# Kernel optimization log

Hardware: AMD Instinct MI355X
Metric: run time of the kernel (lower is better)

## Reference

```python
import jax, jax.numpy as jnp
import numpy as np

DN = ('NCDHW', 'OIDHW', 'NCDHW')


def conv3(x, w):
    # 3x3x3 'same' conv (submanifold conv on a dense volume == padded dense conv)
    return jax.lax.conv_general_dilated(x, w, (1, 1, 1), [(1, 1)] * 3, dimension_numbers=DN)


def conv1(x, w):
    # 1x1x1 conv
    return jax.lax.conv_general_dilated(x, w, (1, 1, 1), 'VALID', dimension_numbers=DN)


def avg_pool(x, ksz):
    s = jax.lax.reduce_window(x, 0.0, jax.lax.add, (1, 1) + ksz, (1, 1) + ksz, 'VALID')
    return s / float(np.prod(ksz))


def setup_inputs() -> dict:
    key = jax.random.key(0)
    ks = jax.random.split(key, 14)
    B, C, D, H, W = 1, 64, 48, 64, 128
    n_dense = 5  # nconvs - 1

    def he(k, shape, fan):
        return jax.random.normal(k, shape, jnp.float32) * np.sqrt(2.0 / fan).astype(np.float32)

    return {
        'fvl': jax.random.normal(ks[0], (B, C, D, H, W), jnp.float32),
        'w_a1': he(ks[1], (C, C, 3, 3, 3), 27 * C),
        'w_a2': he(ks[2], (C, C, 3, 3, 3), 27 * C),
        'w_nin': he(ks[3], (C, C, 1, 1, 1), C),
        'w1s': he(ks[4], (n_dense, C, C, 1, 1, 1), C),
        'w2s': he(ks[5], (n_dense, C, C, 1, 1, 1), C),
        'wp0': he(ks[6], (C, C, 1, 1, 1), C),
        'wp1': he(ks[7], (C, C, 1, 1, 1), C),
        'wp2': he(ks[8], (C, C, 1, 1, 1), C),
        'wp3': he(ks[9], (C, C, 1, 1, 1), C),
        'wc1': he(ks[10], (C, C, 3, 3, 3), 27 * C),
        'wc2': he(ks[11], (1, C, 3, 3, 3), 27 * 1),
        'bc': jnp.zeros((1,), jnp.float32),
    }


def reference(fvl, w_a1, w_a2, w_nin, w1s, w2s, wp0, wp1, wp2, wp3, wc1, wc2, bc):
    # --- Conv3dBlock_sparse: (conv3 -> conv3) + NIN(1x1), summed (no relu) ---
    x = conv3(conv3(fvl, w_a1), w_a2) + conv1(fvl, w_nin)
    # --- (nconvs-1) dense 1x1x1 residual blocks: relu(conv1(x) + conv2(conv1(x))) ---
    for i in range(w1s.shape[0]):
        x1 = conv1(x, w1s[i])
        x2 = conv1(x1, w2s[i])
        x = jax.nn.relu(x1 + x2)
    # --- PSP-style multi-scale pool pyramid ---
    B, C, d, h, w = x.shape
    pool_ws = [wp0, wp1, wp2, wp3]
    out_sum = x
    for i, ps in enumerate(np.linspace(1, min(d, h, w) // 2, 4, dtype=int)):
        ksz = (int(d / ps), int(h / ps), int(w / ps))
        o = avg_pool(x, ksz)
        o = conv1(o, pool_ws[i])
        o = jax.image.resize(o, (B, C, d, h, w), method='trilinear')  # align_corners=False semantics
        out_sum = out_sum + 0.25 * o
    x = jax.nn.relu(out_sum / 2.0)
    # --- classify head (eval path, up=False): conv3 -> relu -> conv3(+bias) ---
    c = conv3(jax.nn.relu(conv3(x, wc1)), wc2) + bc.reshape(1, -1, 1, 1, 1)
    return (x, jnp.squeeze(c, 1))
```

## Files before the change

### kernel.cpp

```cpp
#include <hip/hip_runtime.h>
#include <math.h>

#define DD 48
#define HH 64
#define WW 128
#define VOL (DD*HH*WW)
#define PW 130
#define PROWS (DD*HH)
#define PVOL (PROWS*PW)
#define PVBYTES ((long)PVOL*64*2)
#define GUARD 16640L
#define NC 64

typedef __attribute__((ext_vector_type(8))) short bf16x8;
typedef __attribute__((ext_vector_type(4))) float f32x4;
typedef __attribute__((ext_vector_type(4))) unsigned int u32x4v;
typedef __attribute__((ext_vector_type(2))) unsigned int u32x2v;

__device__ __forceinline__ float bflo(unsigned int u){
    union { unsigned int i; float f; } x; x.i = u<<16; return x.f; }
__device__ __forceinline__ float bfhi(unsigned int u){
    union { unsigned int i; float f; } x; x.i = u & 0xffff0000u; return x.f; }
__device__ __forceinline__ float bf2f(unsigned short u){
    union { unsigned int i; float f; } x; x.i = ((unsigned int)u)<<16; return x.f; }
__device__ __forceinline__ unsigned short f2bf(float f){
    union { float f; unsigned int i; } x; x.f = f;
    unsigned int i = x.i;
    return (unsigned short)((i + 0x7fffu + ((i>>16)&1u)) >> 16);
}

__device__ __forceinline__ void gload16(const void* g, void* l){
    __builtin_amdgcn_global_load_lds(
        (const __attribute__((address_space(1))) void*)g,
        (__attribute__((address_space(3))) void*)l, 16, 0, 0);
}

__global__ void k_prep_all(
    const float* __restrict__ w_a1, const float* __restrict__ w_a2,
    const float* __restrict__ wc1,  const float* __restrict__ wnin,
    const float* __restrict__ wc2,  const float* __restrict__ w1s,
    const float* __restrict__ w2s,  const float* __restrict__ wp1,
    const float* __restrict__ wp2,  const float* __restrict__ wp3,
    unsigned short* __restrict__ wa1t, unsigned short* __restrict__ wa2t,
    unsigned short* __restrict__ wc1t, unsigned short* __restrict__ nint,
    unsigned short* __restrict__ wt2,  unsigned short* __restrict__ Mt,
    float* __restrict__ wpt)
{
    int b = blockIdx.x, tid = threadIdx.x;
    if (b < 1296){
        int which = b/432, bb = b - which*432;
        int idx = bb*256 + tid;
        if (idx < 27*64*64){
            const float* src = which==0 ? w_a1 : (which==1 ? w_a2 : wc1);
            unsigned short* dst = which==0 ? wa1t : (which==1 ? wa2t : wc1t);
            int ci = idx & 63; int t = idx >> 6; int co = t & 63; int k = t >> 6;
            dst[idx] = f2bf(src[(co*64+ci)*27 + k]);
        }
    } else if (b < 1376){
        int idx = (b-1296)*256 + tid;
        int i = idx >> 12; int r = idx & 4095;
        int co = r >> 6; int ci = r & 63;
        const float* W1 = w1s + i*4096;
        const float* W2 = w2s + i*4096;
        float m = W1[co*64+ci];
        for (int k=0;k<64;++k) m += W2[co*64+k]*W1[k*64+ci];
        Mt[idx] = f2bf(m);
    } else if (b < 1392){
        int idx = (b-1376)*256 + tid;
        nint[idx] = f2bf(wnin[idx]);
    } else if (b < 1400){
        int idx = (b-1392)*256 + tid;
        int co = idx & 63; int row = idx >> 6;
        float v = (row < 27) ? wc2[co*27 + row] : 0.f;
        wt2[row*64 + co] = f2bf(v);
    } else {
        int bb = b - 1400;
        int which = bb/16;
        int idx = (bb - which*16)*256 + tid;
        const float* src = which==0 ? wp1 : (which==1 ? wp2 : wp3);
        int ci = idx >> 6; int co = idx & 63;
        wpt[which*4096 + idx] = src[co*64+ci];
    }
}

__global__ __launch_bounds__(256) void k_zeropad(unsigned short* __restrict__ pv0,
                                                 unsigned short* __restrict__ pv1){
    int idx = blockIdx.x*256 + threadIdx.x;
    int seg = idx >> 3, part = idx & 7;
    int vol = seg / 6144; int r2 = seg - vol*6144;
    int row = r2 >> 1; int col = (r2 & 1) ? 129 : 0;
    long boff = ((long)row*130 + col)*128 + part*16;
    u32x4v z = {0,0,0,0};
    char* base = (char*)(vol ? pv1 : pv0);
    *(u32x4v*)(base + boff) = z;
}

__global__ __launch_bounds__(256) void k_tobf16v(const float* __restrict__ src,
                                                 unsigned short* __restrict__ dst){
    __shared__ unsigned short lds[64*66];
    int tid = threadIdx.x;
    long vbase = (long)blockIdx.x*64;
    int d = (int)(vbase >> 13);
    int h = (int)((vbase >> 7) & 63);
    int w0 = (int)(vbase & 127);
    long pbase = ((long)(d*64+h)*PW + w0 + 1);
    int v = tid & 63;
    int cg = tid >> 6;
#pragma unroll
    for (int k=0;k<16;++k){
        int ci = cg*16 + k;
        lds[v*66 + ci] = f2bf(src[(long)ci*VOL + vbase + v]);
    }
    __syncthreads();
#pragma unroll
    for (int it=0; it<2; ++it){
        int chunk = it*256 + tid;
        int vv = chunk >> 3, gp = chunk & 7;
        const unsigned short* s = lds + vv*66 + gp*8;
        unsigned int w0_ = (unsigned)s[0] | ((unsigned)s[1]<<16);
        unsigned int w1_ = (unsigned)s[2] | ((unsigned)s[3]<<16);
        unsigned int w2_ = (unsigned)s[4] | ((unsigned)s[5]<<16);
        unsigned int w3_ = (unsigned)s[6] | ((unsigned)s[7]<<16);
        u32x4v q = {w0_,w1_,w2_,w3_};
        *(u32x4v*)(dst + (pbase+vv)*64 + gp*8) = q;
    }
}

template<bool AUX, bool RELU>
__global__ __launch_bounds__(256,2) void k_conv3m(
    const unsigned short* __restrict__ in, const unsigned short* __restrict__ wt,
    const unsigned short* __restrict__ aux, const unsigned short* __restrict__ auxw,
    unsigned short* __restrict__ out)
{
    __shared__ __align__(16) char sA[36864];
    __shared__ __align__(16) char sB[33280];

    const int tid  = threadIdx.x;
    const int lane = tid & 63;
    const int wave = tid >> 6;
    const int ll = lane & 15;
    const int kg = lane >> 4;
    const int bid = blockIdx.x;
    const int wid = ((bid & 7) * 192) + (bid >> 3);
    const int vbr = wid*256;
    const int d  = vbr >> 13;
    const int h0 = (vbr >> 7) & 63;
    const int my_h  = h0 + (wave >> 1);
    const int my_w0 = (wave & 1) * 64;
    const long pvb = (long)(d*64 + my_h)*PW + my_w0 + 1;

    const char* inb = (const char*)in;
    const char* wtb = (const char*)wt;

    f32x4 acc[4][4];
#pragma unroll
    for (int a=0;a<4;++a)
#pragma unroll
        for (int b=0;b<4;++b) acc[a][b] = (f32x4){0.f,0.f,0.f,0.f};

#pragma unroll
    for (int kd=0; kd<3; ++kd){
        const int dd = d + kd - 1;
        if ((unsigned)dd >= 48u) continue;
        const long rowstart = ((long)(dd*64 + h0 - 1)) * 130;
#pragma unroll
        for (int khalf=0; khalf<2; ++khalf){
            __syncthreads();
#pragma unroll
            for (int rnd=0; rnd<9; ++rnd){
                int j = rnd*4096 + tid*16;
                int q = j ^ (((j>>7)&3)<<4);
                const char* src = wtb + (long)(kd*9 + (q>>12))*8192
                                      + (long)((q>>6)&63)*128 + khalf*64 + (q&63);
                gload16(src, sA + j);
            }
#pragma unroll
            for (int rnd=0; rnd<8; ++rnd){
                int j = rnd*4096 + tid*16;
                int q = j ^ (((j>>7)&3)<<4);
                const char* src = inb + (rowstart + (q>>6))*128 + khalf*64 + (q&63);
                gload16(src, sB + j);
            }
            if (tid < 32){
                int j = 32768 + tid*16;
                int q = j ^ (((j>>7)&3)<<4);
                const char* src = inb + (rowstart + (q>>6))*128 + khalf*64 + (q&63);
                gload16(src, sB + j);
            }
            __syncthreads();
#pragma unroll
            for (int kh=0; kh<3; ++kh){
                const int hh = my_h + kh - 1;
                if ((unsigned)hh >= 64u) continue;
                const int rr = (wave>>1) + kh;
#pragma unroll
                for (int kw=0; kw<3; ++kw){
                    const int tap_rel = kh*3 + kw;
                    bf16x8 Af[4], Bf[4];
#pragma unroll
                    for (int t=0;t<4;++t){
                        int qa = tap_rel*4096 + (t*16+ll)*64 + kg*16;
                        Af[t] = *(const bf16x8*)(sA + (qa ^ (((qa>>7)&3)<<4)));
                    }
#pragma unroll
                    for (int vt=0; vt<4; ++vt){
                        int vrel = rr*130 + my_w0 + vt*16 + ll + kw;
                        int qb = vrel*64 + kg*16;
                        Bf[vt] = *(const bf16x8*)(sB + (qb ^ (((qb>>7)&3)<<4)));
                    }
#pragma unroll
                    for (int vt=0; vt<4; ++vt)
#pragma unroll
                        for (int t=0; t<4; ++t)
                            acc[t][vt] = __builtin_amdgcn_mfma_f32_16x16x32_bf16(Af[t], Bf[vt], acc[t][vt], 0,0,0);
                }
            }
        }
    }

    if (AUX){
        bf16x8 Aa[2][4], Ba[2][4];
#pragma unroll
        for (int half=0; half<2; ++half){
            const int ko = half*32 + kg*8;
#pragma unroll
            for (int t=0;t<4;++t)
                Aa[half][t] = *(const bf16x8*)(auxw + (t*16+ll)*64 + ko);
#pragma unroll
            for (int vt=0; vt<4; ++vt)
                Ba[half][vt] = *(const bf16x8*)(aux + (pvb + vt*16 + ll)*64 + ko);
        }
#pragma unroll
        for (int half=0; half<2; ++half)
#pragma unroll
            for (int vt=0; vt<4; ++vt)
#pragma unroll
                for (int t=0;t<4;++t)
                    acc[t][vt] = __builtin_amdgcn_mfma_f32_16x16x32_bf16(Aa[half][t], Ba[half][vt], acc[t][vt], 0,0,0);
    }

#pragma unroll
    for (int vt=0; vt<4; ++vt){
        unsigned short* op = out + (pvb + vt*16 + ll)*64 + kg*4;
#pragma unroll
        for (int t=0;t<4;++t){
            float r0 = acc[t][vt][0], r1 = acc[t][vt][1], r2 = acc[t][vt][2], r3 = acc[t][vt][3];
            if (RELU){ r0=fmaxf(r0,0.f); r1=fmaxf(r1,0.f); r2=fmaxf(r2,0.f); r3=fmaxf(r3,0.f); }
            unsigned int lo = (unsigned)f2bf(r0) | ((unsigned)f2bf(r1)<<16);
            unsigned int hi = (unsigned)f2bf(r2) | ((unsigned)f2bf(r3)<<16);
            u32x2v q = {lo, hi};
            *(u32x2v*)(op + t*16) = q;
        }
    }
}

__global__ __launch_bounds__(256,2) void k_conv3h(
    const unsigned short* __restrict__ in, const unsigned short* __restrict__ wt,
    const unsigned short* __restrict__ wt2, unsigned short* __restrict__ t)
{
    __shared__ __align__(16) char sA[36864];
    __shared__ __align__(16) char sB[33280];

    const int tid  = threadIdx.x;
    const int lane = tid & 63;
    const int wave = tid >> 6;
    const int ll = lane & 15;
    const int kg = lane >> 4;
    const int bid = blockIdx.x;
    const int wid = ((bid & 7) * 192) + (bid >> 3);
    const int vbr = wid*256;
    const int d  = vbr >> 13;
    const int h0 = (vbr >> 7) & 63;
    const int my_h  = h0 + (wave >> 1);
    const int my_w0 = (wave & 1) * 64;
    const long pvb = (long)(d*64 + my_h)*PW + my_w0 + 1;

    const char* inb = (const char*)in;
    const char* wtb = (const char*)wt;

    f32x4 acc[4][4];
#pragma unroll
    for (int a=0;a<4;++a)
#pragma unroll
        for (int b=0;b<4;++b) acc[a][b] = (f32x4){0.f,0.f,0.f,0.f};

#pragma unroll
    for (int kd=0; kd<3; ++kd){
        const int dd = d + kd - 1;
        if ((unsigned)dd >= 48u) continue;
        const long rowstart = ((long)(dd*64 + h0 - 1)) * 130;
#pragma unroll
        for (int khalf=0; khalf<2; ++khalf){
            __syncthreads();
#pragma unroll
            for (int rnd=0; rnd<9; ++rnd){
                int j = rnd*4096 + tid*16;
                int q = j ^ (((j>>7)&3)<<4);
                const char* src = wtb + (long)(kd*9 + (q>>12))*8192
                                      + (long)((q>>6)&63)*128 + khalf*64 + (q&63);
                gload16(src, sA + j);
            }
#pragma unroll
            for (int rnd=0; rnd<8; ++rnd){
                int j = rnd*4096 + tid*16;
                int q = j ^ (((j>>7)&3)<<4);
                const char* src = inb + (rowstart + (q>>6))*128 + khalf*64 + (q&63);
                gload16(src, sB + j);
            }
            if (tid < 32){
                int j = 32768 + tid*16;
                int q = j ^ (((j>>7)&3)<<4);
                const char* src = inb + (rowstart + (q>>6))*128 + khalf*64 + (q&63);
                gload16(src, sB + j);
            }
            __syncthreads();
#pragma unroll
            for (int kh=0; kh<3; ++kh){
                const int hh = my_h + kh - 1;
                if ((unsigned)hh >= 64u) continue;
                const int rr = (wave>>1) + kh;
#pragma unroll
                for (int kw=0; kw<3; ++kw){
                    const int tap_rel = kh*3 + kw;
                    bf16x8 Af[4], Bf[4];
#pragma unroll
                    for (int tt=0;tt<4;++tt){
                        int qa = tap_rel*4096 + (tt*16+ll)*64 + kg*16;
                        Af[tt] = *(const bf16x8*)(sA + (qa ^ (((qa>>7)&3)<<4)));
                    }
#pragma unroll
                    for (int vt=0; vt<4; ++vt){
                        int vrel = rr*130 + my_w0 + vt*16 + ll + kw;
                        int qb = vrel*64 + kg*16;
                        Bf[vt] = *(const bf16x8*)(sB + (qb ^ (((qb>>7)&3)<<4)));
                    }
#pragma unroll
                    for (int vt=0; vt<4; ++vt)
#pragma unroll
                        for (int tt=0; tt<4; ++tt)
                            acc[tt][vt] = __builtin_amdgcn_mfma_f32_16x16x32_bf16(Af[tt], Bf[vt], acc[tt][vt], 0,0,0);
                }
            }
        }
    }

    __syncthreads();
    char* myL = sA + wave*8192;
#pragma unroll
    for (int vt=0; vt<4; ++vt){
        const int row = vt*16 + ll;
        const int sw = (row & 7) << 4;
#pragma unroll
        for (int tt=0;tt<4;++tt){
            float r0 = fmaxf(acc[tt][vt][0],0.f), r1 = fmaxf(acc[tt][vt][1],0.f);
            float r2 = fmaxf(acc[tt][vt][2],0.f), r3 = fmaxf(acc[tt][vt][3],0.f);
            unsigned int lo = (unsigned)f2bf(r0) | ((unsigned)f2bf(r1)<<16);
            unsigned int hi = (unsigned)f2bf(r2) | ((unsigned)f2bf(r3)<<16);
            u32x2v q = {lo, hi};
            int colb = kg*8 + tt*32;
            *(u32x2v*)(myL + row*128 + (colb ^ sw)) = q;
        }
    }
    f32x4 acc2[2][4];
#pragma unroll
    for (int a=0;a<2;++a)
#pragma unroll
        for (int b=0;b<4;++b) acc2[a][b] = (f32x4){0.f,0.f,0.f,0.f};
#pragma unroll
    for (int half=0; half<2; ++half){
        const int ko = half*32 + kg*8;
        bf16x8 afr[2];
#pragma unroll
        for (int tl=0;tl<2;++tl)
            afr[tl] = *(const bf16x8*)(wt2 + (tl*16+ll)*64 + ko);
#pragma unroll
        for (int vt=0; vt<4; ++vt){
            const int row = vt*16 + ll;
            const int sw = (row & 7) << 4;
            int colb = half*64 + kg*16;
            bf16x8 bfr = *(const bf16x8*)(myL + row*128 + (colb ^ sw));
#pragma unroll
            for (int tl=0;tl<2;++tl)
                acc2[tl][vt] = __builtin_amdgcn_mfma_f32_16x16x32_bf16(afr[tl], bfr, acc2[tl][vt], 0,0,0);
        }
    }
#pragma unroll
    for (int vt=0; vt<4; ++vt){
        long vx = pvb + vt*16 + ll;
#pragma unroll
        for (int tl=0;tl<2;++tl){
#pragma unroll
            for (int r=0;r<4;++r){
                int tap = tl*16 + kg*4 + r;
                if (tap < 27) t[(long)tap*PVOL + vx] = f2bf(acc2[tl][vt][r]);
            }
        }
    }
}

__global__ __launch_bounds__(256,3) void k_chain(const unsigned short* __restrict__ in,
        const unsigned short* __restrict__ Mt, unsigned short* __restrict__ out){
    __shared__ __align__(16) char sX[4][8192];
    const int lane = threadIdx.x & 63;
    const int wave = threadIdx.x >> 6;
    const int ll = lane & 15;
    const int kg = lane >> 4;
    const long vb = (long)blockIdx.x*256 + wave*64;
    char* myL = sX[wave];

    bf16x8 B[2][4];
#pragma unroll
    for (int half=0; half<2; ++half){
        const int ko = half*32 + kg*8;
#pragma unroll
        for (int vt=0; vt<4; ++vt)
            B[half][vt] = *(const bf16x8*)(in + (vb+vt*16+ll)*64 + ko);
    }

#pragma unroll
    for (int s=0; s<5; ++s){
        const unsigned short* wt = Mt + s*4096;
        bf16x8 A[2][4];
#pragma unroll
        for (int half=0; half<2; ++half){
            const int ko = half*32 + kg*8;
#pragma unroll
            for (int t=0;t<4;++t)
                A[half][t] = *(const bf16x8*)(wt + (t*16+ll)*64 + ko);
        }
        f32x4 acc[4][4];
#pragma unroll
        for (int a=0;a<4;++a)
#pragma unroll
            for (int b=0;b<4;++b) acc[a][b] = (f32x4){0.f,0.f,0.f,0.f};
#pragma unroll
        for (int half=0; half<2; ++half)
#pragma unroll
            for (int vt=0; vt<4; ++vt)
#pragma unroll
                for (int t=0;t<4;++t)
                    acc[t][vt] = __builtin_amdgcn_mfma_f32_16x16x32_bf16(A[half][t], B[half][vt], acc[t][vt], 0,0,0);

        if (s < 4){
#pragma unroll
            for (int vt=0; vt<4; ++vt){
                const int row = vt*16 + ll;
                const int sw = (row & 7) << 4;
#pragma unroll
                for (int t=0;t<4;++t){
                    float r0 = fmaxf(acc[t][vt][0],0.f), r1 = fmaxf(acc[t][vt][1],0.f);
                    float r2 = fmaxf(acc[t][vt][2],0.f), r3 = fmaxf(acc[t][vt][3],0.f);
                    unsigned int lo = (unsigned)f2bf(r0) | ((unsigned)f2bf(r1)<<16);
                    unsigned int hi = (unsigned)f2bf(r2) | ((unsigned)f2bf(r3)<<16);
                    u32x2v q = {lo, hi};
                    int colb = kg*8 + t*32;
                    *(u32x2v*)(myL + row*128 + (colb ^ sw)) = q;
                }
            }
#pragma unroll
            for (int half=0; half<2; ++half){
#pragma unroll
                for (int vt=0; vt<4; ++vt){
                    const int row = vt*16 + ll;
                    const int sw = (row & 7) << 4;
                    int colb = half*64 + kg*16;
                    B[half][vt] = *(const bf16x8*)(myL + row*128 + (colb ^ sw));
                }
            }
        } else {
#pragma unroll
            for (int vt=0; vt<4; ++vt){
                unsigned short* op = out + (vb+vt*16+ll)*64 + kg*4;
#pragma unroll
                for (int t=0;t<4;++t){
                    float r0 = fmaxf(acc[t][vt][0],0.f), r1 = fmaxf(acc[t][vt][1],0.f);
                    float r2 = fmaxf(acc[t][vt][2],0.f), r3 = fmaxf(acc[t][vt][3],0.f);
                    unsigned int lo = (unsigned)f2bf(r0) | ((unsigned)f2bf(r1)<<16);
                    unsigned int hi = (unsigned)f2bf(r2) | ((unsigned)f2bf(r3)<<16);
                    u32x2v q = {lo, hi};
                    *(u32x2v*)(op + t*16) = q;
                }
            }
        }
    }
}

__global__ __launch_bounds__(256) void k_heads(const unsigned short* __restrict__ t,
        const float* __restrict__ bias, float* __restrict__ out){
    int g = blockIdx.x*256 + threadIdx.x;
    int v0 = g*4;
    int w0 = v0 & 127; int h = (v0>>7)&63; int d = v0>>13;
    long p0 = (long)(d*64+h)*PW + w0 + 1;
    float b0 = bias[0];
    float s0=b0, s1=b0, s2=b0, s3=b0;
#pragma unroll
    for (int kd=0;kd<3;++kd){
#pragma unroll
      for (int kh=0;kh<3;++kh){
#pragma unroll
        for (int kw=0;kw<3;++kw){
            const int tap = (kd*3+kh)*3+kw;
            const long dvp = (long)((kd-1)*64 + (kh-1))*PW + (kw-1);
            bool okdh = ((unsigned)(d+kd-1)<48u) && ((unsigned)(h+kh-1)<64u);
            const unsigned short* tp = t + (long)tap*PVOL;
            bool ok0 = okdh && ((unsigned)(w0+0+kw-1)<128u);
            bool ok1 = okdh && ((unsigned)(w0+1+kw-1)<128u);
            bool ok2 = okdh && ((unsigned)(w0+2+kw-1)<128u);
            bool ok3 = okdh && ((unsigned)(w0+3+kw-1)<128u);
            long a0 = ok0 ? (p0+0+dvp) : p0;
            long a1 = ok1 ? (p0+1+dvp) : p0;
            long a2 = ok2 ? (p0+2+dvp) : p0;
            long a3 = ok3 ? (p0+3+dvp) : p0;
            float x0 = bf2f(tp[a0]);
            float x1 = bf2f(tp[a1]);
            float x2 = bf2f(tp[a2]);
            float x3 = bf2f(tp[a3]);
            s0 += ok0 ? x0 : 0.f;
            s1 += ok1 ? x1 : 0.f;
            s2 += ok2 ? x2 : 0.f;
            s3 += ok3 ? x3 : 0.f;
        }
      }
    }
    f32x4 r = {s0,s1,s2,s3};
    *(f32x4*)(out + v0) = r;
}

__global__ __launch_bounds__(256) void k_pool3(const unsigned short* __restrict__ in,
                                               float* __restrict__ S3){
    __shared__ float sm[32*68];
    int tid = threadIdx.x;
    int cg = tid & 7, part = tid >> 3;
    int cell = blockIdx.x;
    int Z = cell >> 8, Y = (cell >> 4) & 15, X = cell & 15;
    float a[8];
#pragma unroll
    for (int j=0;j<8;++j) a[j]=0.f;
#pragma unroll
    for (int j=0;j<3;++j){
        int i = part*3 + j;
        int di = i >> 5, rem = i & 31, hi = rem >> 3, wi = rem & 7;
        long p = ((long)((3*Z+di)*64 + 4*Y+hi))*PW + 8*X+wi + 1;
        u32x4v q = *(const u32x4v*)(in + p*64 + cg*8);
#pragma unroll
        for (int e=0;e<4;++e){ a[e*2] += bflo(q[e]); a[e*2+1] += bfhi(q[e]); }
    }
#pragma unroll
    for (int j=0;j<8;++j) sm[part*68 + cg*8 + j] = a[j];
    __syncthreads();
    if (tid < 64){
        float s=0.f;
        for (int r=0;r<32;++r) s += sm[r*68 + tid];
        S3[tid*4096 + cell] = s;
    }
}

__global__ __launch_bounds__(256) void k_pool2(const float* __restrict__ S3,
                                               float* __restrict__ P2){
    int idx = blockIdx.x*256 + threadIdx.x;
    int cell = idx & 511; int c = idx >> 9;
    int z = cell >> 6, y = (cell >> 3) & 7, x = cell & 7;
    const float* b = S3 + c*4096;
    float s = 0.f;
#pragma unroll
    for (int a2=0;a2<2;++a2)
#pragma unroll
        for (int b2=0;b2<2;++b2)
#pragma unroll
            for (int e=0;e<2;++e)
                s += b[((2*z+a2)<<8) + ((2*y+b2)<<4) + (2*x+e)];
    P2[c*512 + cell] = s;
}

__global__ void k_gcm(const float* __restrict__ S3, const float* __restrict__ wp0,
                      float* __restrict__ gc){
    __shared__ float sm[4][64];
    __shared__ float sg[64];
    int tid = threadIdx.x;
    int c = tid & 63, part = tid >> 6;
    float s = 0.f;
    const float* row = S3 + c*4096 + part*1024;
    for (int i=0;i<1024;i+=4){
        f32x4 q = *(const f32x4*)(row + i);
        s += q[0]+q[1]+q[2]+q[3];
    }
    sm[part][c] = s;
    __syncthreads();
    if (tid < 64){
        sg[tid] = (sm[0][tid]+sm[1][tid]+sm[2][tid]+sm[3][tid]) * (1.0f/(float)VOL);
    }
    __syncthreads();
    if (tid < 64){
        float g=0.f;
        for (int ci=0;ci<64;++ci) g += wp0[tid*64+ci]*sg[ci];
        gc[tid] = g;
    }
}

__global__ __launch_bounds__(256) void k_pool4(const unsigned short* __restrict__ in,
                                               float* __restrict__ P4){
    __shared__ float sm[32*68];
    int tid = threadIdx.x;
    int cg = tid & 7, part = (tid >> 3) & 3, slot = tid >> 5;
    int cell = blockIdx.x*8 + slot;
    int z = cell / 800; int rem = cell - z*800; int y = rem / 25; int x = rem - y*25;
    int a2 = part >> 1, b2 = part & 1;
    float a[8];
#pragma unroll
    for (int j=0;j<8;++j) a[j]=0.f;
#pragma unroll
    for (int e=0;e<5;++e){
        long p = ((long)((2*z+a2)*64 + 2*y+b2))*PW + 5*x+e + 1;
        u32x4v q = *(const u32x4v*)(in + p*64 + cg*8);
#pragma unroll
        for (int k=0;k<4;++k){ a[k*2] += bflo(q[k]); a[k*2+1] += bfhi(q[k]); }
    }
#pragma unroll
    for (int j=0;j<8;++j) sm[(slot*4+part)*68 + cg*8 + j] = a[j];
    __syncthreads();
#pragma unroll
    for (int r=0;r<2;++r){
        int o = r*256 + tid;
        int c = o >> 3, s = o & 7;
        float v = sm[(s*4+0)*68 + c] + sm[(s*4+1)*68 + c]
                + sm[(s*4+2)*68 + c] + sm[(s*4+3)*68 + c];
        P4[(long)c*19200 + blockIdx.x*8 + s] = v;
    }
}

__global__ void k_conv1(const float* __restrict__ in, const float* __restrict__ wt,
                        float* __restrict__ out, int vol, float scale){
    int v = blockIdx.x*256 + threadIdx.x;
    if (v >= vol) return;
    float acc[64];
#pragma unroll
    for (int i=0;i<64;++i) acc[i]=0.f;
    for (int ci=0; ci<64; ++ci){
        float xv = in[ci*vol + v];
        const float* wr = wt + ci*64;
#pragma unroll
        for (int co=0; co<64; ++co) acc[co] = fmaf(wr[co], xv, acc[co]);
    }
    float* op = out + (long)v*64;
#pragma unroll
    for (int q=0;q<16;++q){
        f32x4 t = {acc[q*4]*scale, acc[q*4+1]*scale, acc[q*4+2]*scale, acc[q*4+3]*scale};
        *(f32x4*)(op + q*4) = t;
    }
}

__device__ __forceinline__ void tri_setup(int d,int h,int w,int gd,int gh,int gw,
                                          int* o, float* wt){
    float fz = (d+0.5f)*((float)gd/(float)DD) - 0.5f;
    float fy = (h+0.5f)*((float)gh/(float)HH) - 0.5f;
    float fx = (w+0.5f)*((float)gw/(float)WW) - 0.5f;
    float z0f = floorf(fz), y0f = floorf(fy), x0f = floorf(fx);
    float tz = fz - z0f, ty = fy - y0f, tx = fx - x0f;
    int z0 = (int)z0f, y0 = (int)y0f, x0 = (int)x0f;
    int z1 = z0+1, y1 = y0+1, x1 = x0+1;
    z0 = min(max(z0,0),gd-1); z1 = min(max(z1,0),gd-1);
    y0 = min(max(y0,0),gh-1); y1 = min(max(y1,0),gh-1);
    x0 = min(max(x0,0),gw-1); x1 = min(max(x1,0),gw-1);
    o[0] = (z0*gh+y0)*gw+x0; wt[0] = (1-tz)*(1-ty)*(1-tx);
    o[1] = (z0*gh+y0)*gw+x1; wt[1] = (1-tz)*(1-ty)*tx;
    o[2] = (z0*gh+y1)*gw+x0; wt[2] = (1-tz)*ty*(1-tx);
    o[3] = (z0*gh+y1)*gw+x1; wt[3] = (1-tz)*ty*tx;
    o[4] = (z1*gh+y0)*gw+x0; wt[4] = tz*(1-ty)*(1-tx);
    o[5] = (z1*gh+y0)*gw+x1; wt[5] = tz*(1-ty)*tx;
    o[6] = (z1*gh+y1)*gw+x0; wt[6] = tz*ty*(1-tx);
    o[7] = (z1*gh+y1)*gw+x1; wt[7] = tz*ty*tx;
}

__global__ __launch_bounds__(512) void k_combine(
        const unsigned short* __restrict__ xc, const float* __restrict__ gc,
        const float* __restrict__ p2, const float* __restrict__ p3,
        const float* __restrict__ p4, float* __restrict__ xout,
        unsigned short* __restrict__ xv){
    int tid = threadIdx.x;
    const int bid = blockIdx.x;
    const int wid = ((bid & 7) * 96) + (bid >> 3);
    long v = (long)wid*512 + tid;
    int w = v & 127; int h = (v>>7)&63; int d = v>>13;
    long p = (long)(d*64+h)*PW + w + 1;
    int o2[8], o3[8], o4[8];
    float w2_[8], w3_[8], w4_[8];
    tri_setup(d,h,w, 8,8,8,    o2, w2_);
    tri_setup(d,h,w, 16,16,16, o3, w3_);
    tri_setup(d,h,w, 24,32,25, o4, w4_);
#pragma unroll
    for (int half=0; half<2; ++half){
        float res[32];
#pragma unroll
        for (int j=0;j<32;++j) res[j] = gc[half*32+j];
#pragma unroll
        for (int t=0;t<8;++t){
            const float* b2 = p2 + (long)o2[t]*64 + half*32;
#pragma unroll
            for (int q=0;q<8;++q){
                f32x4 x4 = *(const f32x4*)(b2 + q*4);
                res[q*4+0] = fmaf(w2_[t], x4[0], res[q*4+0]);
                res[q*4+1] = fmaf(w2_[t], x4[1], res[q*4+1]);
                res[q*4+2] = fmaf(w2_[t], x4[2], res[q*4+2]);
                res[q*4+3] = fmaf(w2_[t], x4[3], res[q*4+3]);
            }
        }
#pragma unroll
        for (int t=0;t<8;++t){
            const float* b3 = p3 + (long)o3[t]*64 + half*32;
#pragma unroll
            for (int q=0;q<8;++q){
                f32x4 x4 = *(const f32x4*)(b3 + q*4);
                res[q*4+0] = fmaf(w3_[t], x4[0], res[q*4+0]);
                res[q*4+1] = fmaf(w3_[t], x4[1], res[q*4+1]);
                res[q*4+2] = fmaf(w3_[t], x4[2], res[q*4+2]);
                res[q*4+3] = fmaf(w3_[t], x4[3], res[q*4+3]);
            }
        }
#pragma unroll
        for (int t=0;t<8;++t){
            const float* b4 = p4 + (long)o4[t]*64 + half*32;
#pragma unroll
            for (int q=0;q<8;++q){
                f32x4 x4 = *(const f32x4*)(b4 + q*4);
                res[q*4+0] = fmaf(w4_[t], x4[0], res[q*4+0]);
                res[q*4+1] = fmaf(w4_[t], x4[1], res[q*4+1]);
                res[q*4+2] = fmaf(w4_[t], x4[2], res[q*4+2]);
                res[q*4+3] = fmaf(w4_[t], x4[3], res[q*4+3]);
            }
        }
        const u32x4v* xq = (const u32x4v*)(xc + p*64 + half*32);
#pragma unroll
        for (int q=0;q<4;++q){
            u32x4v qv = xq[q];
            unsigned int pk[4];
#pragma unroll
            for (int e=0;e<4;++e){
                int j = q*8 + e*2;
                float r0 = fmaxf((bflo(qv[e]) + 0.25f*res[j])*0.5f, 0.f);
                float r1 = fmaxf((bfhi(qv[e]) + 0.25f*res[j+1])*0.5f, 0.f);
                __builtin_nontemporal_store(r0, &xout[(long)(half*32+j)*VOL + v]);
                __builtin_nontemporal_store(r1, &xout[(long)(half*32+j+1)*VOL + v]);
                pk[e] = (unsigned)f2bf(r0) | ((unsigned)f2bf(r1)<<16);
            }
            u32x4v pq = {pk[0],pk[1],pk[2],pk[3]};
            *(u32x4v*)(xv + p*64 + half*32 + q*8) = pq;
        }
    }
}

constexpr long RPV = GUARD + PVBYTES + GUARD;
constexpr long OFF_PV0R = 0;
constexpr long OFF_PV1R = RPV;
constexpr long OFF_WA1 = 2*RPV;
constexpr long OFF_WA2 = OFF_WA1 + 221184;
constexpr long OFF_WC1 = OFF_WA2 + 221184;
constexpr long OFF_NIN = OFF_WC1 + 221184;
constexpr long OFF_MT  = OFF_NIN + 8192;
constexpr long OFF_WT2 = OFF_MT + 40960;
constexpr long OFF_WPT = OFF_WT2 + 4096;
constexpr long OFF_GC  = OFF_WPT + 49152;
constexpr long OFF_P2  = OFF_GC + 256;
constexpr long OFF_P2C = OFF_P2 + 131072;
constexpr long OFF_S3  = OFF_P2C + 131072;
constexpr long OFF_P3C = OFF_S3 + 1048576;
constexpr long OFF_P4  = OFF_P3C + 1048576;
constexpr long OFF_P4C = OFF_P4 + 4915200;

extern "C" void kernel_launch(void* const* d_in, const int* in_sizes, int n_in,
                              void* d_out, int out_size, void* d_ws, size_t ws_size,
                              hipStream_t stream) {
    const float* fvl  = (const float*)d_in[0];
    const float* w_a1 = (const float*)d_in[1];
    const float* w_a2 = (const float*)d_in[2];
    const float* wnin = (const float*)d_in[3];
    const float* w1s  = (const float*)d_in[4];
    const float* w2s  = (const float*)d_in[5];
    const float* wp0  = (const float*)d_in[6];
    const float* wp1  = (const float*)d_in[7];
    const float* wp2  = (const float*)d_in[8];
    const float* wp3  = (const float*)d_in[9];
    const float* wc1  = (const float*)d_in[10];
    const float* wc2  = (const float*)d_in[11];
    const float* bc   = (const float*)d_in[12];

    char* ws = (char*)d_ws;
    unsigned short* PV0  = (unsigned short*)(ws + OFF_PV0R + GUARD);
    unsigned short* PV1  = (unsigned short*)(ws + OFF_PV1R + GUARD);
    unsigned short* wa1t = (unsigned short*)(ws + OFF_WA1);
    unsigned short* wa2t = (unsigned short*)(ws + OFF_WA2);
    unsigned short* wc1t = (unsigned short*)(ws + OFF_WC1);
    unsigned short* nint = (unsigned short*)(ws + OFF_NIN);
    unsigned short* Mt   = (unsigned short*)(ws + OFF_MT);
    unsigned short* wt2  = (unsigned short*)(ws + OFF_WT2);
    float* wpt  = (float*)(ws + OFF_WPT);
    float* gc   = (float*)(ws + OFF_GC);
    float* p2   = (float*)(ws + OFF_P2);
    float* p2c  = (float*)(ws + OFF_P2C);
    float* S3   = (float*)(ws + OFF_S3);
    float* p3c  = (float*)(ws + OFF_P3C);
    float* p4   = (float*)(ws + OFF_P4);
    float* p4c  = (float*)(ws + OFF_P4C);

    float* Xout = (float*)d_out;
    float* Cout = Xout + (long)NC*VOL;
    unsigned short* Tbuf = PV1;

    const int GBR = VOL/256;
    const int GBP = PVOL/256;

    k_zeropad<<<384,256,0,stream>>>(PV0, PV1);

    k_prep_all<<<1448,256,0,stream>>>(w_a1, w_a2, wc1, wnin, wc2, w1s, w2s,
                                      wp1, wp2, wp3,
                                      wa1t, wa2t, wc1t, nint, wt2, Mt, wpt);
    k_tobf16v<<<VOL/64,256,0,stream>>>(fvl, PV0);

    k_conv3m<false,false><<<GBR,256,0,stream>>>(PV0, wa1t, nullptr, nullptr, PV1);
    k_conv3m<true,false><<<GBR,256,0,stream>>>(PV1, wa2t, PV0, nint, PV0);

    k_chain<<<GBP,256,0,stream>>>(PV0, Mt, PV1);

    k_pool3<<<4096,256,0,stream>>>(PV1, S3);
    k_gcm<<<1,256,0,stream>>>(S3, wp0, gc);
    k_pool2<<<128,256,0,stream>>>(S3, p2);
    k_pool4<<<2400,256,0,stream>>>(PV1, p4);
    k_conv1<<<2,256,0,stream>>>(p2, wpt + 0*4096, p2c, 512,   1.0f/768.0f);
    k_conv1<<<16,256,0,stream>>>(S3, wpt + 1*4096, p3c, 4096, 1.0f/96.0f);
    k_conv1<<<75,256,0,stream>>>(p4, wpt + 2*4096, p4c, 19200, 1.0f/20.0f);

    k_combine<<<768,512,0,stream>>>(PV1, gc, p2c, p3c, p4c, Xout, PV0);

    k_conv3h<<<GBR,256,0,stream>>>(PV0, wc1t, wt2, Tbuf);
    k_heads<<<384,256,0,stream>>>(Tbuf, bc, Cout);
}
```

Baseline: 584.5 us.

## Split fp32 output store from combine into separate LDS transpose kernel

The combine kernel now writes only the bf16 channels-last volume and runs with 256-thread blocks. A new kernel reads that bf16 volume back, transposes it through LDS and writes the fp32 channel-major output with 16-byte nontemporal stores. This replaces 64 scalar strided stores per thread in combine with wide vector stores. In exchange it adds a kernel launch and an extra full read of the bf16 volume. The fp32 output is also now rounded to bf16 precision.

```diff
diff --git a/kernel.cpp b/kernel.cpp
--- a/kernel.cpp
+++ b/kernel.cpp
@@ -671,15 +671,14 @@
     o[7] = (z1*gh+y1)*gw+x1; wt[7] = tz*ty*tx;
 }
 
-__global__ __launch_bounds__(512) void k_combine(
+__global__ __launch_bounds__(256) void k_combine(
         const unsigned short* __restrict__ xc, const float* __restrict__ gc,
         const float* __restrict__ p2, const float* __restrict__ p3,
-        const float* __restrict__ p4, float* __restrict__ xout,
-        unsigned short* __restrict__ xv){
+        const float* __restrict__ p4, unsigned short* __restrict__ xv){
     int tid = threadIdx.x;
     const int bid = blockIdx.x;
-    const int wid = ((bid & 7) * 96) + (bid >> 3);
-    long v = (long)wid*512 + tid;
+    const int wid = ((bid & 7) * 192) + (bid >> 3);
+    long v = (long)wid*256 + tid;
     int w = v & 127; int h = (v>>7)&63; int d = v>>13;
     long p = (long)(d*64+h)*PW + w + 1;
     int o2[8], o3[8], o4[8];
@@ -738,13 +737,48 @@
                 int j = q*8 + e*2;
                 float r0 = fmaxf((bflo(qv[e]) + 0.25f*res[j])*0.5f, 0.f);
                 float r1 = fmaxf((bfhi(qv[e]) + 0.25f*res[j+1])*0.5f, 0.f);
-                __builtin_nontemporal_store(r0, &xout[(long)(half*32+j)*VOL + v]);
-                __builtin_nontemporal_store(r1, &xout[(long)(half*32+j+1)*VOL + v]);
                 pk[e] = (unsigned)f2bf(r0) | ((unsigned)f2bf(r1)<<16);
             }
             u32x4v pq = {pk[0],pk[1],pk[2],pk[3]};
             *(u32x4v*)(xv + p*64 + half*32 + q*8) = pq;
         }
+    }
+}
+
+__global__ __launch_bounds__(256) void k_xpose(const unsigned short* __restrict__ xv,
+                                               float* __restrict__ xout){
+    __shared__ unsigned int lds32[32][261];
+    int tid = threadIdx.x;
+    const int bid = blockIdx.x;
+    const int wid = ((bid & 7) * 192) + (bid >> 3);
+    long vb = (long)wid*256;
+    {
+        long gv = vb + tid;
+        int row = (int)(gv >> 7); int w = (int)(gv & 127);
+        long p = (long)row*PW + w + 1;
+        const u32x4v* src = (const u32x4v*)(xv + p*64);
+#pragma unroll
+        for (int g=0; g<8; ++g){
+            u32x4v q = src[g];
+#pragma unroll
+            for (int e=0;e<4;++e)
+                lds32[g*4+e][tid] = q[e];
+        }
+    }
+    __syncthreads();
+    int c = tid & 63, part = tid >> 6;
+    int cp = c >> 1; bool hiw = (c & 1);
+    int v0 = part*64;
+    float* op = xout + (long)c*VOL + vb + v0;
+#pragma unroll
+    for (int k=0;k<16;++k){
+        f32x4 o;
+#pragma unroll
+        for (int e=0;e<4;++e){
+            unsigned int u = lds32[cp][v0 + k*4 + e];
+            o[e] = hiw ? bfhi(u) : bflo(u);
+        }
+        __builtin_nontemporal_store(o, (f32x4*)(op + k*4));
     }
 }
 
@@ -828,7 +862,8 @@
     k_conv1<<<16,256,0,stream>>>(S3, wpt + 1*4096, p3c, 4096, 1.0f/96.0f);
     k_conv1<<<75,256,0,stream>>>(p4, wpt + 2*4096, p4c, 19200, 1.0f/20.0f);
 
-    k_combine<<<768,512,0,stream>>>(PV1, gc, p2c, p3c, p4c, Xout, PV0);
+    k_combine<<<GBR,256,0,stream>>>(PV1, gc, p2c, p3c, p4c, PV0);
+    k_xpose<<<GBR,256,0,stream>>>(PV0, Xout);
 
     k_conv3h<<<GBR,256,0,stream>>>(PV0, wc1t, wt2, Tbuf);
     k_heads<<<384,256,0,stream>>>(Tbuf, bc, Cout);
```

Result: slower. 880.3 us (+50.6%).
